# Performance work log

Measured on AMD Instinct MI355X. Metric: run time of the kernel, lower is better.

## Reference

```python
import jax, jax.numpy as jnp
import numpy as np

B, N, D_IN, D_OUT = 4, 4096, 512, 256
ALPHA = 0.2          # LeakyReLU negative slope
NEG_BIG = -9e15      # value used to mask non-edges before softmax


def setup_inputs() -> dict:
    key = jax.random.key(0)
    k_h, k_adj, k_w, k_a = jax.random.split(key, 4)
    h = jax.random.normal(k_h, (B, N, D_IN), dtype=jnp.float32)
    adj = jax.random.randint(k_adj, (N, N), 0, 2, dtype=jnp.int32)
    # xavier_uniform with gain 1.414
    lim_w = 1.414 * np.sqrt(6.0 / (D_IN + D_OUT))
    Ws = jax.random.uniform(k_w, (B, D_IN, D_OUT), jnp.float32, -lim_w, lim_w)
    lim_a = 1.414 * np.sqrt(6.0 / (2 * D_OUT + 1))
    a = jax.random.uniform(k_a, (B, 2 * D_OUT, 1), jnp.float32, -lim_a, lim_a)
    return {"h": h, "adj": adj, "Ws": Ws, "a": a}


def reference(h, adj, Ws, a):
    d_out = Ws.shape[-1]
    Wh = jnp.einsum('bni,bio->bno', h, Ws)                 # [B,N,D_OUT]
    a1 = a[:, :d_out, 0]                                    # [B,D_OUT]
    a2 = a[:, d_out:, 0]                                    # [B,D_OUT]
    e1 = jnp.einsum('bno,bo->bn', Wh, a1)                   # [B,N]
    e2 = jnp.einsum('bno,bo->bn', Wh, a2)                   # [B,N]
    e = e1[:, :, None] + e2[:, None, :]                     # [B,N,N]
    e = jnp.where(e > 0, e, ALPHA * e)                      # LeakyReLU
    scores = jnp.where(adj[None, :, :] > 0, e, NEG_BIG)     # mask non-edges
    att = jax.nn.softmax(scores, axis=-1)                   # over neighbors j
    # dropout omitted (eval mode / p irrelevant for correctness baseline)
    h_prime = jnp.einsum('bnm,bmo->bno', att, Wh)           # [B,N,D_OUT]
    return jax.nn.elu(h_prime)                              # concat=True -> elu
```

## Files before the change

### kernel.cpp

```cpp
#include <hip/hip_runtime.h>
#include <hip/hip_bf16.h>
#include <stdint.h>

#define B_    4
#define NN    4096
#define DIN   512
#define DOUT  256
#define ALPHA_ 0.2f

typedef __attribute__((ext_vector_type(8))) short short8;
typedef __attribute__((ext_vector_type(4))) float f32x4;
typedef __attribute__((ext_vector_type(2))) float f32x2;

typedef const __attribute__((address_space(1))) void gconst_void;
typedef __attribute__((address_space(3))) void lds_void;

__device__ __forceinline__ unsigned short f2bf(float x) {
    union { float f; uint32_t u; } v; v.f = x;
    uint32_t r = v.u + 0x7FFFu + ((v.u >> 16) & 1u);
    return (unsigned short)(r >> 16);
}

__global__ __launch_bounds__(256) void k_prep(const int* __restrict__ adj,
                                              const float4* __restrict__ h4,
                                              const float* __restrict__ Ws,
                                              uint32_t* __restrict__ bits,
                                              uint2* __restrict__ hb,
                                              unsigned short* __restrict__ wst) {
    const int gt = blockIdx.x * 256 + threadIdx.x;
    const int NT = 2048 * 256;
    for (int idx = gt; idx < NN * NN; idx += NT) {
        unsigned long long m = __ballot(adj[idx] > 0);
        if ((threadIdx.x & 63) == 0)
            *reinterpret_cast<unsigned long long*>(bits + ((idx >> 6) << 1)) = m;
    }
    for (int idx = gt; idx < B_ * NN * DIN / 4; idx += NT) {
        float4 v = h4[idx];
        uint2 o;
        o.x = (uint32_t)f2bf(v.x) | ((uint32_t)f2bf(v.y) << 16);
        o.y = (uint32_t)f2bf(v.z) | ((uint32_t)f2bf(v.w) << 16);
        hb[idx] = o;
    }
    for (int idx = gt; idx < B_ * DOUT * DIN; idx += NT) {
        int k = idx & (DIN - 1);
        int o = (idx >> 9) & (DOUT - 1);
        int b = idx >> 17;
        wst[idx] = f2bf(Ws[((size_t)b * DIN + k) * DOUT + o]);
    }
}

__global__ __launch_bounds__(256) void k_gemm1(const unsigned short* __restrict__ hb,
                                               const unsigned short* __restrict__ wst,
                                               const float* __restrict__ a,
                                               unsigned short* __restrict__ wht,
                                               float2* __restrict__ x1t,
                                               float* __restrict__ y1t,
                                               float* __restrict__ y2t) {
    __shared__ unsigned short Ah[64 * 64];
    __shared__ unsigned short Bw[256 * 64];
    __shared__ float e1s[64], e2s[64];
    const int tid = threadIdx.x;
    const int w = tid >> 6, lane = tid & 63;
    const int l15 = lane & 15, lhi = lane >> 4;
    const int b = blockIdx.y;
    const int n0 = blockIdx.x * 64;
    const unsigned short* hrow = hb + ((size_t)b * NN + n0) * DIN;
    const unsigned short* wrow = wst + (size_t)b * DOUT * DIN;

    if (tid < 64) { e1s[tid] = 0.f; e2s[tid] = 0.f; }

    f32x4 acc[4][4] = {};

    for (int kt = 0; kt < DIN / 64; ++kt) {
        const int k0 = kt * 64;
        #pragma unroll
        for (int it = 0; it < 2; ++it) {
            int q = it * 256 + tid;
            int row = q >> 3, c = q & 7;
            const unsigned short* src = hrow + (size_t)row * DIN + k0 + 8 * (c ^ (row & 7));
            char* dst = reinterpret_cast<char*>(Ah) + it * 4096 + w * 1024;
            __builtin_amdgcn_global_load_lds((gconst_void*)src, (lds_void*)dst, 16, 0, 0);
        }
        #pragma unroll
        for (int it = 0; it < 8; ++it) {
            int q = it * 256 + tid;
            int row = q >> 3, c = q & 7;
            const unsigned short* src = wrow + (size_t)row * DIN + k0 + 8 * (c ^ (row & 7));
            char* dst = reinterpret_cast<char*>(Bw) + it * 4096 + w * 1024;
            __builtin_amdgcn_global_load_lds((gconst_void*)src, (lds_void*)dst, 16, 0, 0);
        }
        __syncthreads();
        #pragma unroll
        for (int kk = 0; kk < 2; ++kk) {
            short8 af[4], bfr[4];
            #pragma unroll
            for (int rf = 0; rf < 4; ++rf) {
                int row = rf * 16 + l15;
                int off = row * 128 + ((kk * 64 + lhi * 16) ^ ((row & 7) << 4));
                af[rf] = *reinterpret_cast<const short8*>(reinterpret_cast<const char*>(Ah) + off);
            }
            #pragma unroll
            for (int cf = 0; cf < 4; ++cf) {
                int row = w * 64 + cf * 16 + l15;
                int off = row * 128 + ((kk * 64 + lhi * 16) ^ ((row & 7) << 4));
                bfr[cf] = *reinterpret_cast<const short8*>(reinterpret_cast<const char*>(Bw) + off);
            }
            #pragma unroll
            for (int rf = 0; rf < 4; ++rf)
                #pragma unroll
                for (int cf = 0; cf < 4; ++cf)
                    acc[rf][cf] = __builtin_amdgcn_mfma_f32_16x16x32_bf16(af[rf], bfr[cf], acc[rf][cf], 0, 0, 0);
        }
        __syncthreads();
    }
    unsigned short* wb = wht + (size_t)b * DOUT * NN;
    #pragma unroll
    for (int rf = 0; rf < 4; ++rf) {
        #pragma unroll
        for (int cf = 0; cf < 4; ++cf) {
            int d = w * 64 + cf * 16 + l15;
            int m = n0 + rf * 16 + lhi * 4;
            uint2 pk;
            pk.x = (uint32_t)f2bf(acc[rf][cf][0]) | ((uint32_t)f2bf(acc[rf][cf][1]) << 16);
            pk.y = (uint32_t)f2bf(acc[rf][cf][2]) | ((uint32_t)f2bf(acc[rf][cf][3]) << 16);
            *reinterpret_cast<uint2*>(wb + (size_t)d * NN + m) = pk;
        }
    }
    const float* ab = a + b * 2 * DOUT;
    float a1v[4], a2v[4];
    #pragma unroll
    for (int cf = 0; cf < 4; ++cf) {
        int d = w * 64 + cf * 16 + l15;
        a1v[cf] = ab[d];
        a2v[cf] = ab[DOUT + d];
    }
    #pragma unroll
    for (int rf = 0; rf < 4; ++rf) {
        #pragma unroll
        for (int j = 0; j < 4; ++j) {
            float p1 = 0.f, p2 = 0.f;
            #pragma unroll
            for (int cf = 0; cf < 4; ++cf) {
                p1 = fmaf(acc[rf][cf][j], a1v[cf], p1);
                p2 = fmaf(acc[rf][cf][j], a2v[cf], p2);
            }
            #pragma unroll
            for (int msk = 1; msk < 16; msk <<= 1) {
                p1 += __shfl_xor(p1, msk);
                p2 += __shfl_xor(p2, msk);
            }
            if (l15 == 0) {
                atomicAdd(&e1s[rf * 16 + lhi * 4 + j], p1);
                atomicAdd(&e2s[rf * 16 + lhi * 4 + j], p2);
            }
        }
    }
    __syncthreads();
    if (tid < 64) {
        float e1v = e1s[tid], e2v = e2s[tid];
        x1t[b * NN + n0 + tid] = float2{__expf(e1v), __expf(ALPHA_ * e1v)};
        y1t[b * NN + n0 + tid] = __expf(e2v);
        y2t[b * NN + n0 + tid] = __expf(ALPHA_ * e2v);
    }
}

__global__ __launch_bounds__(512, 4) void k_attn(const unsigned short* __restrict__ wht,
                                                 const uint32_t* __restrict__ bits,
                                                 const float2* __restrict__ x1t,
                                                 const float* __restrict__ y1t,
                                                 const float* __restrict__ y2t,
                                                 float* __restrict__ out,
                                                 float* __restrict__ sums) {
    __shared__ unsigned short Bw[2 * 256 * 64];
    __shared__ unsigned short Pt[64 * 64];

    const int tid = threadIdx.x;
    const int w = tid >> 6, lane = tid & 63;
    const int l15 = lane & 15, lh4 = lane >> 4;
    const int wn = w >> 2, wd = w & 3;

    const int bid = blockIdx.x;
    const int wg = ((bid & 7) << 6) | (bid >> 3);
    const int g  = wg >> 6;
    const int b  = g >> 1;
    const int n0 = ((g & 1) * 32 + (wg & 31)) << 6;
    const int T0 = ((wg >> 5) & 1) * 32;

    const int pr = tid >> 3, pc = tid & 7;
    const float2 xv = x1t[b * NN + n0 + pr];
    const float X1 = xv.x, X2 = xv.y;
    const unsigned short* wb = wht + (size_t)b * DOUT * NN;

    f32x4 acc[2][4] = {};
    f32x4 accs[2] = {};
    short8 ones;
    {
        union { short8 v; uint32_t u[4]; } ov;
        ov.u[0] = 0x3F803F80u; ov.u[1] = 0x3F803F80u;
        ov.u[2] = 0x3F803F80u; ov.u[3] = 0x3F803F80u;
        ones = ov.v;
    }

    const unsigned short* sp[4];
    #pragma unroll
    for (int it = 0; it < 4; ++it) {
        int q = it * 512 + tid;
        int row = q >> 3, c = q & 7;
        sp[it] = wb + (size_t)row * NN + T0 * 64 + 8 * (c ^ (row & 7));
    }
    const uint8_t* bp = reinterpret_cast<const uint8_t*>(bits) +
                        (size_t)(n0 + pr) * (NN / 8) + T0 * 8 + pc;
    const float4* y1p = reinterpret_cast<const float4*>(y1t + b * NN + T0 * 64 + pc * 8);
    const float4* y2p = reinterpret_cast<const float4*>(y2t + b * NN + T0 * 64 + pc * 8);

#define STAGE(BUF)                                                                     \
    {                                                                                  \
        _Pragma("unroll")                                                              \
        for (int it = 0; it < 4; ++it) {                                               \
            char* dst = reinterpret_cast<char*>(Bw) + (BUF) * 32768 + it * 8192 + w * 1024; \
            __builtin_amdgcn_global_load_lds((gconst_void*)sp[it], (lds_void*)dst, 16, 0, 0); \
            sp[it] += 64;                                                              \
        }                                                                              \
    }

#define P_MATH(BB, Y1A, Y1B, Y2A, Y2B, PKW)                                            \
    {                                                                                  \
        float v1[8] = {Y1A.x, Y1A.y, Y1A.z, Y1A.w, Y1B.x, Y1B.y, Y1B.z, Y1B.w};        \
        float v2[8] = {Y2A.x, Y2A.y, Y2A.z, Y2A.w, Y2B.x, Y2B.y, Y2B.z, Y2B.w};        \
        _Pragma("unroll")                                                              \
        for (int i = 0; i < 4; ++i) {                                                  \
            f32x2 pa = f32x2{v1[2 * i], v1[2 * i + 1]} * X1;                           \
            f32x2 pb = f32x2{v2[2 * i], v2[2 * i + 1]} * X2;                           \
            f32x2 pm = __builtin_elementwise_max(pa, pb);                              \
            union { __hip_bfloat162 h; uint32_t u; } cc;                               \
            cc.h = __float22bfloat162_rn(float2{pm.x, pm.y});                          \
            uint32_t b2 = ((BB) >> (2 * i)) & 3u;                                      \
            uint32_t mk = ((b2 & 1u) ? 0xFFFFu : 0u) | ((b2 & 2u) ? 0xFFFF0000u : 0u); \
            PKW[i] = cc.u & mk;                                                        \
        }                                                                              \
    }

#define PT_WRITE(PKW)                                                                  \
    {                                                                                  \
        uint4 qv; qv.x = PKW[0]; qv.y = PKW[1]; qv.z = PKW[2]; qv.w = PKW[3];          \
        *reinterpret_cast<uint4*>(reinterpret_cast<char*>(Pt) + pr * 128 +             \
                                  ((pc * 16) ^ ((pr & 7) << 4))) = qv;                 \
    }

#define MM(CUR)                                                                        \
    {                                                                                  \
        const char* bwb = reinterpret_cast<const char*>(Bw) + (CUR) * 32768;           \
        const char* ptb = reinterpret_cast<const char*>(Pt);                           \
        __builtin_amdgcn_s_setprio(1);                                                 \
        _Pragma("unroll")                                                              \
        for (int kk = 0; kk < 2; ++kk) {                                               \
            short8 af[2], bf[4];                                                       \
            _Pragma("unroll")                                                          \
            for (int rf = 0; rf < 2; ++rf) {                                           \
                int row = wn * 32 + rf * 16 + l15;                                     \
                int off = row * 128 + ((kk * 64 + lh4 * 16) ^ ((row & 7) << 4));       \
                af[rf] = *reinterpret_cast<const short8*>(ptb + off);                  \
            }                                                                          \
            _Pragma("unroll")                                                          \
            for (int cf = 0; cf < 4; ++cf) {                                           \
                int row = wd * 64 + cf * 16 + l15;                                     \
                int off = row * 128 + ((kk * 64 + lh4 * 16) ^ ((row & 7) << 4));       \
                bf[cf] = *reinterpret_cast<const short8*>(bwb + off);                  \
            }                                                                          \
            _Pragma("unroll")                                                          \
            for (int rf = 0; rf < 2; ++rf) {                                           \
                _Pragma("unroll")                                                      \
                for (int cf = 0; cf < 4; ++cf)                                         \
                    acc[rf][cf] = __builtin_amdgcn_mfma_f32_16x16x32_bf16(             \
                        af[rf], bf[cf], acc[rf][cf], 0, 0, 0);                         \
                accs[rf] = __builtin_amdgcn_mfma_f32_16x16x32_bf16(                    \
                    af[rf], ones, accs[rf], 0, 0, 0);                                  \
            }                                                                          \
        }                                                                              \
        __builtin_amdgcn_s_setprio(0);                                                 \
    }

    STAGE(0)
    {
        uint32_t bb = *bp; bp += 8;
        float4 y1a = y1p[0], y1b = y1p[1]; y1p += 16;
        float4 y2a = y2p[0], y2b = y2p[1]; y2p += 16;
        uint32_t pkw[4];
        P_MATH(bb, y1a, y1b, y2a, y2b, pkw)
        PT_WRITE(pkw)
    }
    __syncthreads();

    for (int t = 0; t < 32; ++t) {
        const int cur = t & 1;
        uint32_t pkw[4];
        if (t < 31) {
            STAGE(cur ^ 1)
            uint32_t bb = *bp; bp += 8;
            float4 y1a = y1p[0], y1b = y1p[1]; y1p += 16;
            float4 y2a = y2p[0], y2b = y2p[1]; y2p += 16;
            P_MATH(bb, y1a, y1b, y2a, y2b, pkw)
        }
        MM(cur)
        __syncthreads();
        if (t < 31) {
            PT_WRITE(pkw)
            __syncthreads();
        }
    }
#undef STAGE
#undef P_MATH
#undef PT_WRITE
#undef MM

    #pragma unroll
    for (int rf = 0; rf < 2; ++rf) {
        #pragma unroll
        for (int cf = 0; cf < 4; ++cf) {
            int d = wd * 64 + cf * 16 + l15;
            #pragma unroll
            for (int j = 0; j < 4; ++j) {
                int nr = n0 + wn * 32 + rf * 16 + lh4 * 4 + j;
                atomicAdd(&out[((size_t)b * NN + nr) * DOUT + d], acc[rf][cf][j]);
            }
        }
    }
    if (wd == 0 && l15 == 0) {
        #pragma unroll
        for (int rf = 0; rf < 2; ++rf)
            #pragma unroll
            for (int j = 0; j < 4; ++j) {
                int nr = n0 + wn * 32 + rf * 16 + lh4 * 4 + j;
                atomicAdd(&sums[b * NN + nr], accs[rf][j]);
            }
    }
}

__global__ __launch_bounds__(256) void k_final(const float* __restrict__ sums,
                                               float* __restrict__ out) {
    int f4 = blockIdx.x * 256 + threadIdx.x;
    int row = f4 >> 6;
    float inv = 1.0f / sums[row];
    float4 v = reinterpret_cast<const float4*>(out)[f4];
    v.x *= inv; v.y *= inv; v.z *= inv; v.w *= inv;
    v.x = v.x > 0.f ? v.x : (__expf(v.x) - 1.f);
    v.y = v.y > 0.f ? v.y : (__expf(v.y) - 1.f);
    v.z = v.z > 0.f ? v.z : (__expf(v.z) - 1.f);
    v.w = v.w > 0.f ? v.w : (__expf(v.w) - 1.f);
    reinterpret_cast<float4*>(out)[f4] = v;
}

extern "C" void kernel_launch(void* const* d_in, const int* in_sizes, int n_in,
                              void* d_out, int out_size, void* d_ws, size_t ws_size,
                              hipStream_t stream) {
    (void)in_sizes; (void)n_in; (void)out_size; (void)ws_size;
    const float* h   = (const float*)d_in[0];
    const int*   adj = (const int*)d_in[1];
    const float* Ws  = (const float*)d_in[2];
    const float* a   = (const float*)d_in[3];
    float* out = (float*)d_out;

    char* ws = (char*)d_ws;
    unsigned short* hb  = (unsigned short*)(ws);
    unsigned short* wst = (unsigned short*)(ws + 16777216);
    unsigned short* wht = (unsigned short*)(ws + 17825792);
    float2* x1t = (float2*)(ws + 26214400);
    float*  y1t = (float*)(ws + 26345472);
    float*  y2t = (float*)(ws + 26411008);
    uint32_t* bits = (uint32_t*)(ws + 26476544);
    float* sums = (float*)(ws + 28573696);

    hipMemsetAsync(out, 0, (size_t)B_ * NN * DOUT * sizeof(float), stream);
    hipMemsetAsync(sums, 0, (size_t)B_ * NN * sizeof(float), stream);
    k_prep<<<dim3(2048), dim3(256), 0, stream>>>(adj, (const float4*)h, Ws,
                                                 bits, (uint2*)hb, wst);
    k_gemm1<<<dim3(NN / 64, B_), dim3(256), 0, stream>>>(hb, wst, a, wht, x1t, y1t, y2t);
    k_attn<<<dim3(512), dim3(512), 0, stream>>>(wht, bits, x1t, y1t, y2t, out, sums);
    k_final<<<dim3(B_ * NN * DOUT / 1024), dim3(256), 0, stream>>>(sums, out);
}
```

Measured before the change: 132.3 us.

## Enlarge attention row tile to 128 and compute row sums on vector ALU

```diff
diff --git a/kernel.cpp b/kernel.cpp
--- a/kernel.cpp
+++ b/kernel.cpp
@@ -172,7 +172,7 @@
                                                  float* __restrict__ out,
                                                  float* __restrict__ sums) {
     __shared__ unsigned short Bw[2 * 256 * 64];
-    __shared__ unsigned short Pt[64 * 64];
+    __shared__ unsigned short Pt[128 * 64];
 
     const int tid = threadIdx.x;
     const int w = tid >> 6, lane = tid & 63;
@@ -182,24 +182,18 @@
     const int bid = blockIdx.x;
     const int wg = ((bid & 7) << 6) | (bid >> 3);
     const int g  = wg >> 6;
+    const int r  = wg & 63;
     const int b  = g >> 1;
-    const int n0 = ((g & 1) * 32 + (wg & 31)) << 6;
-    const int T0 = ((wg >> 5) & 1) * 32;
-
-    const int pr = tid >> 3, pc = tid & 7;
+    const int n0 = ((g & 1) * 16 + (r & 15)) << 7;
+    const int T0 = (r >> 4) * 16;
+
+    const int pr = tid >> 2, pc = tid & 3;
     const float2 xv = x1t[b * NN + n0 + pr];
     const float X1 = xv.x, X2 = xv.y;
     const unsigned short* wb = wht + (size_t)b * DOUT * NN;
 
-    f32x4 acc[2][4] = {};
-    f32x4 accs[2] = {};
-    short8 ones;
-    {
-        union { short8 v; uint32_t u[4]; } ov;
-        ov.u[0] = 0x3F803F80u; ov.u[1] = 0x3F803F80u;
-        ov.u[2] = 0x3F803F80u; ov.u[3] = 0x3F803F80u;
-        ones = ov.v;
-    }
+    f32x4 acc[4][4] = {};
+    f32x2 psum2 = {0.f, 0.f};
 
     const unsigned short* sp[4];
     #pragma unroll
@@ -209,9 +203,9 @@
         sp[it] = wb + (size_t)row * NN + T0 * 64 + 8 * (c ^ (row & 7));
     }
     const uint8_t* bp = reinterpret_cast<const uint8_t*>(bits) +
-                        (size_t)(n0 + pr) * (NN / 8) + T0 * 8 + pc;
-    const float4* y1p = reinterpret_cast<const float4*>(y1t + b * NN + T0 * 64 + pc * 8);
-    const float4* y2p = reinterpret_cast<const float4*>(y2t + b * NN + T0 * 64 + pc * 8);
+                        (size_t)(n0 + pr) * (NN / 8) + T0 * 8 + pc * 2;
+    const float4* y1p = reinterpret_cast<const float4*>(y1t + b * NN + T0 * 64 + pc * 16);
+    const float4* y2p = reinterpret_cast<const float4*>(y2t + b * NN + T0 * 64 + pc * 16);
 
 #define STAGE(BUF)                                                                     \
     {                                                                                  \
@@ -223,12 +217,14 @@
         }                                                                              \
     }
 
-#define P_MATH(BB, Y1A, Y1B, Y2A, Y2B, PKW)                                            \
+#define P_MATH(BB, Y1A, Y1B, Y1C, Y1D, Y2A, Y2B, Y2C, Y2D, PKW)                        \
     {                                                                                  \
-        float v1[8] = {Y1A.x, Y1A.y, Y1A.z, Y1A.w, Y1B.x, Y1B.y, Y1B.z, Y1B.w};        \
-        float v2[8] = {Y2A.x, Y2A.y, Y2A.z, Y2A.w, Y2B.x, Y2B.y, Y2B.z, Y2B.w};        \
+        float v1[16] = {Y1A.x, Y1A.y, Y1A.z, Y1A.w, Y1B.x, Y1B.y, Y1B.z, Y1B.w,        \
+                        Y1C.x, Y1C.y, Y1C.z, Y1C.w, Y1D.x, Y1D.y, Y1D.z, Y1D.w};       \
+        float v2[16] = {Y2A.x, Y2A.y, Y2A.z, Y2A.w, Y2B.x, Y2B.y, Y2B.z, Y2B.w,        \
+                        Y2C.x, Y2C.y, Y2C.z, Y2C.w, Y2D.x, Y2D.y, Y2D.z, Y2D.w};       \
         _Pragma("unroll")                                                              \
-        for (int i = 0; i < 4; ++i) {                                                  \
+        for (int i = 0; i < 8; ++i) {                                                  \
             f32x2 pa = f32x2{v1[2 * i], v1[2 * i + 1]} * X1;                           \
             f32x2 pb = f32x2{v2[2 * i], v2[2 * i + 1]} * X2;                           \
             f32x2 pm = __builtin_elementwise_max(pa, pb);                              \
@@ -236,15 +232,21 @@
             cc.h = __float22bfloat162_rn(float2{pm.x, pm.y});                          \
             uint32_t b2 = ((BB) >> (2 * i)) & 3u;                                      \
             uint32_t mk = ((b2 & 1u) ? 0xFFFFu : 0u) | ((b2 & 2u) ? 0xFFFF0000u : 0u); \
-            PKW[i] = cc.u & mk;                                                        \
+            uint32_t q = cc.u & mk;                                                    \
+            PKW[i] = q;                                                                \
+            union { uint32_t u; float f; } qlo, qhi;                                   \
+            qlo.u = q << 16; qhi.u = q & 0xFFFF0000u;                                  \
+            psum2 += f32x2{qlo.f, qhi.f};                                              \
         }                                                                              \
     }
 
 #define PT_WRITE(PKW)                                                                  \
     {                                                                                  \
-        uint4 qv; qv.x = PKW[0]; qv.y = PKW[1]; qv.z = PKW[2]; qv.w = PKW[3];          \
-        *reinterpret_cast<uint4*>(reinterpret_cast<char*>(Pt) + pr * 128 +             \
-                                  ((pc * 16) ^ ((pr & 7) << 4))) = qv;                 \
+        uint4 qa; qa.x = PKW[0]; qa.y = PKW[1]; qa.z = PKW[2]; qa.w = PKW[3];          \
+        uint4 qb; qb.x = PKW[4]; qb.y = PKW[5]; qb.z = PKW[6]; qb.w = PKW[7];          \
+        char* base = reinterpret_cast<char*>(Pt) + pr * 128;                           \
+        *reinterpret_cast<uint4*>(base + ((pc * 32)      ^ ((pr & 7) << 4))) = qa;     \
+        *reinterpret_cast<uint4*>(base + ((pc * 32 + 16) ^ ((pr & 7) << 4))) = qb;     \
     }
 
 #define MM(CUR)                                                                        \
@@ -254,10 +256,10 @@
         __builtin_amdgcn_s_setprio(1);                                                 \
         _Pragma("unroll")                                                              \
         for (int kk = 0; kk < 2; ++kk) {                                               \
-            short8 af[2], bf[4];                                                       \
+            short8 af[4];                                                              \
             _Pragma("unroll")                                                          \
-            for (int rf = 0; rf < 2; ++rf) {                                           \
-                int row = wn * 32 + rf * 16 + l15;                                     \
+            for (int rf = 0; rf < 4; ++rf) {                                           \
+                int row = wn * 64 + rf * 16 + l15;                                     \
                 int off = row * 128 + ((kk * 64 + lh4 * 16) ^ ((row & 7) << 4));       \
                 af[rf] = *reinterpret_cast<const short8*>(ptb + off);                  \
             }                                                                          \
@@ -265,16 +267,11 @@
             for (int cf = 0; cf < 4; ++cf) {                                           \
                 int row = wd * 64 + cf * 16 + l15;                                     \
                 int off = row * 128 + ((kk * 64 + lh4 * 16) ^ ((row & 7) << 4));       \
-                bf[cf] = *reinterpret_cast<const short8*>(bwb + off);                  \
-            }                                                                          \
-            _Pragma("unroll")                                                          \
-            for (int rf = 0; rf < 2; ++rf) {                                           \
+                short8 bf = *reinterpret_cast<const short8*>(bwb + off);               \
                 _Pragma("unroll")                                                      \
-                for (int cf = 0; cf < 4; ++cf)                                         \
+                for (int rf = 0; rf < 4; ++rf)                                         \
                     acc[rf][cf] = __builtin_amdgcn_mfma_f32_16x16x32_bf16(             \
-                        af[rf], bf[cf], acc[rf][cf], 0, 0, 0);                         \
-                accs[rf] = __builtin_amdgcn_mfma_f32_16x16x32_bf16(                    \
-                    af[rf], ones, accs[rf], 0, 0, 0);                                  \
+                        af[rf], bf, acc[rf][cf], 0, 0, 0);                             \
             }                                                                          \
         }                                                                              \
         __builtin_amdgcn_s_setprio(0);                                                 \
@@ -282,28 +279,28 @@
 
     STAGE(0)
     {
-        uint32_t bb = *bp; bp += 8;
-        float4 y1a = y1p[0], y1b = y1p[1]; y1p += 16;
-        float4 y2a = y2p[0], y2b = y2p[1]; y2p += 16;
-        uint32_t pkw[4];
-        P_MATH(bb, y1a, y1b, y2a, y2b, pkw)
+        uint32_t bb = *reinterpret_cast<const uint16_t*>(bp); bp += 8;
+        float4 y1a = y1p[0], y1b = y1p[1], y1c = y1p[2], y1d = y1p[3]; y1p += 16;
+        float4 y2a = y2p[0], y2b = y2p[1], y2c = y2p[2], y2d = y2p[3]; y2p += 16;
+        uint32_t pkw[8];
+        P_MATH(bb, y1a, y1b, y1c, y1d, y2a, y2b, y2c, y2d, pkw)
         PT_WRITE(pkw)
     }
     __syncthreads();
 
-    for (int t = 0; t < 32; ++t) {
+    for (int t = 0; t < 16; ++t) {
         const int cur = t & 1;
-        uint32_t pkw[4];
-        if (t < 31) {
+        uint32_t pkw[8];
+        if (t < 15) {
             STAGE(cur ^ 1)
-            uint32_t bb = *bp; bp += 8;
-            float4 y1a = y1p[0], y1b = y1p[1]; y1p += 16;
-            float4 y2a = y2p[0], y2b = y2p[1]; y2p += 16;
-            P_MATH(bb, y1a, y1b, y2a, y2b, pkw)
+            uint32_t bb = *reinterpret_cast<const uint16_t*>(bp); bp += 8;
+            float4 y1a = y1p[0], y1b = y1p[1], y1c = y1p[2], y1d = y1p[3]; y1p += 16;
+            float4 y2a = y2p[0], y2b = y2p[1], y2c = y2p[2], y2d = y2p[3]; y2p += 16;
+            P_MATH(bb, y1a, y1b, y1c, y1d, y2a, y2b, y2c, y2d, pkw)
         }
         MM(cur)
         __syncthreads();
-        if (t < 31) {
+        if (t < 15) {
             PT_WRITE(pkw)
             __syncthreads();
         }
@@ -313,26 +310,22 @@
 #undef PT_WRITE
 #undef MM
 
-    #pragma unroll
-    for (int rf = 0; rf < 2; ++rf) {
+    float ps = psum2.x + psum2.y;
+    ps += __shfl_xor(ps, 1);
+    ps += __shfl_xor(ps, 2);
+    if (pc == 0) atomicAdd(&sums[b * NN + n0 + pr], ps);
+
+    #pragma unroll
+    for (int rf = 0; rf < 4; ++rf) {
         #pragma unroll
         for (int cf = 0; cf < 4; ++cf) {
             int d = wd * 64 + cf * 16 + l15;
             #pragma unroll
             for (int j = 0; j < 4; ++j) {
-                int nr = n0 + wn * 32 + rf * 16 + lh4 * 4 + j;
+                int nr = n0 + wn * 64 + rf * 16 + lh4 * 4 + j;
                 atomicAdd(&out[((size_t)b * NN + nr) * DOUT + d], acc[rf][cf][j]);
             }
         }
-    }
-    if (wd == 0 && l15 == 0) {
-        #pragma unroll
-        for (int rf = 0; rf < 2; ++rf)
-            #pragma unroll
-            for (int j = 0; j < 4; ++j) {
-                int nr = n0 + wn * 32 + rf * 16 + lh4 * 4 + j;
-                atomicAdd(&sums[b * NN + nr], accs[rf][j]);
-            }
     }
 }
 
```

After: 178.9 us. 35.2% more time.

## Double-buffer P tile and replace atomic accumulation with split partial buffers

Applied to the files above, without the earlier changes.

```diff
diff --git a/kernel.cpp b/kernel.cpp
--- a/kernel.cpp
+++ b/kernel.cpp
@@ -170,9 +170,11 @@
                                                  const float* __restrict__ y1t,
                                                  const float* __restrict__ y2t,
                                                  float* __restrict__ out,
-                                                 float* __restrict__ sums) {
+                                                 float* __restrict__ part1,
+                                                 float* __restrict__ sums0,
+                                                 float* __restrict__ sums1) {
     __shared__ unsigned short Bw[2 * 256 * 64];
-    __shared__ unsigned short Pt[64 * 64];
+    __shared__ unsigned short Pt[2 * 64 * 64];
 
     const int tid = threadIdx.x;
     const int w = tid >> 6, lane = tid & 63;
@@ -240,17 +242,17 @@
         }                                                                              \
     }
 
-#define PT_WRITE(PKW)                                                                  \
+#define PT_WRITE(PKW, BUF)                                                             \
     {                                                                                  \
         uint4 qv; qv.x = PKW[0]; qv.y = PKW[1]; qv.z = PKW[2]; qv.w = PKW[3];          \
-        *reinterpret_cast<uint4*>(reinterpret_cast<char*>(Pt) + pr * 128 +             \
-                                  ((pc * 16) ^ ((pr & 7) << 4))) = qv;                 \
+        *reinterpret_cast<uint4*>(reinterpret_cast<char*>(Pt) + (BUF) * 8192 +         \
+                                  pr * 128 + ((pc * 16) ^ ((pr & 7) << 4))) = qv;      \
     }
 
 #define MM(CUR)                                                                        \
     {                                                                                  \
         const char* bwb = reinterpret_cast<const char*>(Bw) + (CUR) * 32768;           \
-        const char* ptb = reinterpret_cast<const char*>(Pt);                           \
+        const char* ptb = reinterpret_cast<const char*>(Pt) + (CUR) * 8192;            \
         __builtin_amdgcn_s_setprio(1);                                                 \
         _Pragma("unroll")                                                              \
         for (int kk = 0; kk < 2; ++kk) {                                               \
@@ -287,32 +289,30 @@
         float4 y2a = y2p[0], y2b = y2p[1]; y2p += 16;
         uint32_t pkw[4];
         P_MATH(bb, y1a, y1b, y2a, y2b, pkw)
-        PT_WRITE(pkw)
+        PT_WRITE(pkw, 0)
     }
     __syncthreads();
 
     for (int t = 0; t < 32; ++t) {
         const int cur = t & 1;
-        uint32_t pkw[4];
         if (t < 31) {
             STAGE(cur ^ 1)
             uint32_t bb = *bp; bp += 8;
             float4 y1a = y1p[0], y1b = y1p[1]; y1p += 16;
             float4 y2a = y2p[0], y2b = y2p[1]; y2p += 16;
+            uint32_t pkw[4];
             P_MATH(bb, y1a, y1b, y2a, y2b, pkw)
+            PT_WRITE(pkw, cur ^ 1)
         }
         MM(cur)
         __syncthreads();
-        if (t < 31) {
-            PT_WRITE(pkw)
-            __syncthreads();
-        }
     }
 #undef STAGE
 #undef P_MATH
 #undef PT_WRITE
 #undef MM
 
+    float* pdst = (T0 == 0) ? out : part1;
     #pragma unroll
     for (int rf = 0; rf < 2; ++rf) {
         #pragma unroll
@@ -321,28 +321,35 @@
             #pragma unroll
             for (int j = 0; j < 4; ++j) {
                 int nr = n0 + wn * 32 + rf * 16 + lh4 * 4 + j;
-                atomicAdd(&out[((size_t)b * NN + nr) * DOUT + d], acc[rf][cf][j]);
+                pdst[((size_t)b * NN + nr) * DOUT + d] = acc[rf][cf][j];
             }
         }
     }
     if (wd == 0 && l15 == 0) {
+        float* sdst = (T0 == 0) ? sums0 : sums1;
         #pragma unroll
         for (int rf = 0; rf < 2; ++rf)
             #pragma unroll
             for (int j = 0; j < 4; ++j) {
                 int nr = n0 + wn * 32 + rf * 16 + lh4 * 4 + j;
-                atomicAdd(&sums[b * NN + nr], accs[rf][j]);
-            }
-    }
-}
-
-__global__ __launch_bounds__(256) void k_final(const float* __restrict__ sums,
+                sdst[b * NN + nr] = accs[rf][j];
+            }
+    }
+}
+
+__global__ __launch_bounds__(256) void k_final(const float* __restrict__ part1,
+                                               const float* __restrict__ sums0,
+                                               const float* __restrict__ sums1,
                                                float* __restrict__ out) {
     int f4 = blockIdx.x * 256 + threadIdx.x;
     int row = f4 >> 6;
-    float inv = 1.0f / sums[row];
+    float inv = 1.0f / (sums0[row] + sums1[row]);
     float4 v = reinterpret_cast<const float4*>(out)[f4];
-    v.x *= inv; v.y *= inv; v.z *= inv; v.w *= inv;
+    float4 p = reinterpret_cast<const float4*>(part1)[f4];
+    v.x = (v.x + p.x) * inv;
+    v.y = (v.y + p.y) * inv;
+    v.z = (v.z + p.z) * inv;
+    v.w = (v.w + p.w) * inv;
     v.x = v.x > 0.f ? v.x : (__expf(v.x) - 1.f);
     v.y = v.y > 0.f ? v.y : (__expf(v.y) - 1.f);
     v.z = v.z > 0.f ? v.z : (__expf(v.z) - 1.f);
@@ -368,13 +375,14 @@
     float*  y1t = (float*)(ws + 26345472);
     float*  y2t = (float*)(ws + 26411008);
     uint32_t* bits = (uint32_t*)(ws + 26476544);
-    float* sums = (float*)(ws + 28573696);
-
-    hipMemsetAsync(out, 0, (size_t)B_ * NN * DOUT * sizeof(float), stream);
-    hipMemsetAsync(sums, 0, (size_t)B_ * NN * sizeof(float), stream);
+    float* sums0 = (float*)(ws + 28573696);
+    float* sums1 = (float*)(ws + 28639232);
+    float* part1 = (float*)hb;
+
     k_prep<<<dim3(2048), dim3(256), 0, stream>>>(adj, (const float4*)h, Ws,
                                                  bits, (uint2*)hb, wst);
     k_gemm1<<<dim3(NN / 64, B_), dim3(256), 0, stream>>>(hb, wst, a, wht, x1t, y1t, y2t);
-    k_attn<<<dim3(512), dim3(512), 0, stream>>>(wht, bits, x1t, y1t, y2t, out, sums);
-    k_final<<<dim3(B_ * NN * DOUT / 1024), dim3(256), 0, stream>>>(sums, out);
-}
+    k_attn<<<dim3(512), dim3(512), 0, stream>>>(wht, bits, x1t, y1t, y2t,
+                                                out, part1, sums0, sums1);
+    k_final<<<dim3(B_ * NN * DOUT / 1024), dim3(256), 0, stream>>>(part1, sums0, sums1, out);
+}
```

Result: faster. 106.2 us, median of 3 (-19.7%).
